# Kernel tuning notes

Measured on AMD Instinct MI355X. Metric: run time of the kernel, lower is better.

## Reference

```python
import jax, jax.numpy as jnp
import numpy as np

EPS = 0.001  # numerical_stabilizer


def setup_inputs() -> dict:
    key = jax.random.key(0)
    ks = jax.random.split(key, 8)
    B, L, D, H, M = 4, 4096, 1024, 16, 64
    scale = 0.02
    return {
        "query": jax.random.normal(ks[0], (B, L, D), jnp.float32),
        "key": jax.random.normal(ks[1], (B, L, D), jnp.float32),
        "value": jax.random.normal(ks[2], (B, L, D), jnp.float32),
        "Wq": jax.random.normal(ks[3], (D, H, M), jnp.float32) * scale,
        "bq": jnp.zeros((H, M), jnp.float32),
        "Wk": jax.random.normal(ks[4], (D, H, M), jnp.float32) * scale,
        "bk": jnp.zeros((H, M), jnp.float32),
        "Wv": jax.random.normal(ks[5], (D, H, M), jnp.float32) * scale,
        "bv": jnp.zeros((H, M), jnp.float32),
        "Wo": jax.random.normal(ks[6], (H, M, D), jnp.float32) * scale,
        "bo": jnp.zeros((D,), jnp.float32),
        "step": 0,
    }


def reference(query, key, value, Wq, bq, Wk, bk, Wv, bv, Wo, bo, step):
    # QKV projections: [B,L,D] x [D,H,M] -> [B,L,H,M]
    q = jnp.einsum('bld,dhm->blhm', query, Wq) + bq
    k = jnp.einsum('bld,dhm->blhm', key, Wk) + bk
    v = jnp.einsum('bld,dhm->blhm', value, Wv) + bv
    # ReLU feature map with stabilizer
    q = jax.nn.relu(q) + EPS
    k = jax.nn.relu(k) + EPS
    # Linear (kernelized) attention: KV outer-product state [B,H,M,M]
    kvs = jnp.einsum('blhm,blhd->bhmd', k, v)
    a_v = jnp.einsum('blhm,bhmd->blhd', q, kvs)
    # Normalizer: sum of keys over sequence
    ks_sum = jnp.sum(k, axis=1)                       # [B,H,M]
    norm = jnp.einsum('blhm,bhm->blh', q, ks_sum)     # [B,L,H]
    a_v = a_v / norm[..., None]
    # Output projection over (head, head_dim) -> hidden
    out = jnp.einsum('blhm,hmd->bld', a_v, Wo) + bo
    return out
```

## Files before the change

kernel.cpp:

```cpp
#include <hip/hip_runtime.h>
#include <stdint.h>


typedef __bf16 bf16;
typedef __bf16 bf16x4 __attribute__((ext_vector_type(4)));
typedef __bf16 bf16x8 __attribute__((ext_vector_type(8)));
typedef float f32x4 __attribute__((ext_vector_type(4)));

#define MFMA_(a, b, c) __builtin_amdgcn_mfma_f32_16x16x32_bf16((a), (b), (c), 0, 0, 0)

static constexpr int BB   = 4;
static constexpr int LSEQ = 4096;
static constexpr int DIM  = 1024;
static constexpr int HH   = 16;
static constexpr float EPSF = 0.001f;

__device__ __forceinline__ void gload16(bf16* lds, const bf16* g) {
  __builtin_amdgcn_global_load_lds(
      (const __attribute__((address_space(1))) void*)g,
      (__attribute__((address_space(3))) void*)lds, 16, 0, 0);
}

__global__ void k_prep_w4(const float* __restrict__ W0, const float* __restrict__ W1,
                          const float* __restrict__ W2, const float* __restrict__ W3,
                          bf16* __restrict__ T0, bf16* __restrict__ T1,
                          bf16* __restrict__ T2, bf16* __restrict__ T3) {
  const float* W; bf16* T;
  switch (blockIdx.z) {
    case 0:  W = W0; T = T0; break;
    case 1:  W = W1; T = T1; break;
    case 2:  W = W2; T = T2; break;
    default: W = W3; T = T3; break;
  }
  __shared__ float t[32][33];
  const int tx = threadIdx.x & 31, ty = threadIdx.x >> 5;
  const int r0 = blockIdx.x * 32, c0 = blockIdx.y * 32;
#pragma unroll
  for (int j = 0; j < 32; j += 8)
    t[ty + j][tx] = W[(size_t)(r0 + ty + j) * DIM + c0 + tx];
  __syncthreads();
#pragma unroll
  for (int j = 0; j < 32; j += 8)
    T[(size_t)(c0 + ty + j) * DIM + r0 + tx] = (bf16)t[tx][ty + j];
}

__global__ void k_init_vt(bf16* __restrict__ vt) {
  const int c = blockIdx.x * 256 + threadIdx.x;
  const int l8 = c & 511;
  const int r  = (c >> 9) & 15;
  const int bh = c >> 13;
  const bf16 val = (r == 0) ? (bf16)1.0f : (bf16)0.0f;
  bf16x8 o;
#pragma unroll
  for (int j = 0; j < 8; ++j) o[j] = val;
  *reinterpret_cast<bf16x8*>(vt + ((size_t)bh * 80 + 64 + r) * LSEQ + l8 * 8) = o;
}

template <int MODE>
__global__ __launch_bounds__(512, 2) void k_projf(const float* __restrict__ X,
                                                  const bf16* __restrict__ WT,
                                                  const float* __restrict__ bias,
                                                  bf16* __restrict__ outp) {
  __shared__ __align__(16) bf16 SH[65536];
  bf16* As = SH;
  bf16* Bs = SH + 16384;
  const int tid = threadIdx.x;
  const int lane = tid & 63, w = tid >> 6;
  const int wm = w >> 2, wn = w & 3;
  const int lr = lane & 15, lk = (lane >> 4) & 3;
  const int n0 = blockIdx.x * 256, c0 = blockIdx.y * 256;
  const int swz = (lr & 7) * 8;
  const int col0 = (lk * 8) ^ swz;
  const int col1 = (lk * 8 + 32) ^ swz;
  const int srow = lane >> 3;
  const int scol = (((lane & 7) ^ ((lane >> 3) & 7)) * 8);
  const float* Xb = X + (size_t)n0 * DIM;
  const bf16* Bb = WT + (size_t)c0 * DIM;

  f32x4 acc[8][4] = {};
  f32x4 af[8];
  const int arow[1] = {0};  (void)arow;

#pragma unroll
  for (int j = 0; j < 8; ++j) {
    const int idx = tid + j * 512, row = idx >> 4, c4 = idx & 15;
    af[j] = __builtin_nontemporal_load(
        reinterpret_cast<const f32x4*>(Xb + (size_t)row * DIM + c4 * 4));
  }

  for (int ks = 0; ks < 16; ++ks) {
    const int k0 = ks * 64;
    __syncthreads();
#pragma unroll
    for (int rr = 0; rr < 4; ++rr) {
      const int row = (rr * 8 + w) * 8 + srow;
      gload16(Bs + (rr * 8 + w) * 512, Bb + (size_t)row * DIM + k0 + scol);
    }
#pragma unroll
    for (int j = 0; j < 8; ++j) {
      const int idx = tid + j * 512, row = idx >> 4, c4 = idx & 15;
      bf16x4 o;
      o[0] = (bf16)af[j][0]; o[1] = (bf16)af[j][1];
      o[2] = (bf16)af[j][2]; o[3] = (bf16)af[j][3];
      *reinterpret_cast<bf16x4*>(
          &As[row * 64 + ((((c4 >> 1) ^ (row & 7)) << 3) | ((c4 & 1) << 2))]) = o;
    }
    __syncthreads();
    if (ks < 15) {
#pragma unroll
      for (int j = 0; j < 8; ++j) {
        const int idx = tid + j * 512, row = idx >> 4, c4 = idx & 15;
        af[j] = __builtin_nontemporal_load(
            reinterpret_cast<const f32x4*>(Xb + (size_t)row * DIM + k0 + 64 + c4 * 4));
      }
    }
    bf16x8 a[8][2], b[4][2];
#pragma unroll
    for (int f = 0; f < 8; ++f) {
      a[f][0] = *reinterpret_cast<const bf16x8*>(&As[(wm * 128 + f * 16 + lr) * 64 + col0]);
      a[f][1] = *reinterpret_cast<const bf16x8*>(&As[(wm * 128 + f * 16 + lr) * 64 + col1]);
    }
#pragma unroll
    for (int cb = 0; cb < 4; ++cb) {
      b[cb][0] = *reinterpret_cast<const bf16x8*>(&Bs[(wn * 64 + cb * 16 + lr) * 64 + col0]);
      b[cb][1] = *reinterpret_cast<const bf16x8*>(&Bs[(wn * 64 + cb * 16 + lr) * 64 + col1]);
    }
#pragma unroll
    for (int kk = 0; kk < 2; ++kk)
#pragma unroll
      for (int f = 0; f < 8; ++f)
#pragma unroll
        for (int cb = 0; cb < 4; ++cb)
          acc[f][cb] = MFMA_(a[f][kk], b[cb][kk], acc[f][cb]);
  }

  float bvv[4];
#pragma unroll
  for (int cb = 0; cb < 4; ++cb) bvv[cb] = bias[c0 + wn * 64 + cb * 16 + lr];
  const int bidx = n0 >> 12;
  const int l0 = n0 & (LSEQ - 1);

  if (MODE == 0) {
    __syncthreads();
#pragma unroll
    for (int f = 0; f < 8; ++f)
#pragma unroll
      for (int cb = 0; cb < 4; ++cb) {
        const int cl = wn * 64 + cb * 16 + lr;
#pragma unroll
        for (int r = 0; r < 4; ++r) {
          float x = acc[f][cb][r] + bvv[cb];
          x = fmaxf(x, 0.f) + EPSF;
          const int ll = wm * 128 + f * 16 + lk * 4 + r;
          SH[ll * 256 + ((((cl >> 3) ^ (ll & 7)) << 3) | (cl & 7))] = (bf16)x;
        }
      }
    __syncthreads();
#pragma unroll
    for (int it = 0; it < 16; ++it) {
      const int chunk = it * 512 + tid;
      const int row = chunk >> 5, blk = chunk & 31;
      const bf16x8 v = *reinterpret_cast<const bf16x8*>(&SH[row * 256 + ((blk ^ (row & 7)) << 3)]);
      *reinterpret_cast<bf16x8*>(outp + (size_t)(n0 + row) * DIM + c0 + blk * 8) = v;
    }
  } else {
    __syncthreads();
#pragma unroll
    for (int f = 0; f < 8; ++f)
#pragma unroll
      for (int cb = 0; cb < 4; ++cb) {
        const int cl = wn * 64 + cb * 16 + lr;
        const int ll = wm * 128 + f * 16 + lk * 4;
        bf16x4 o;
#pragma unroll
        for (int r = 0; r < 4; ++r) {
          float x = acc[f][cb][r] + bvv[cb];
          if (MODE == 1) x = fmaxf(x, 0.f) + EPSF;
          o[r] = (bf16)x;
        }
        *reinterpret_cast<bf16x4*>(
            &SH[cl * 256 + ((((ll >> 3) ^ (cl & 7)) << 3) | (ll & 7))]) = o;
      }
    __syncthreads();
#pragma unroll
    for (int it = 0; it < 16; ++it) {
      const int chunk = it * 512 + tid;
      const int row = chunk >> 5, blk = chunk & 31;
      const bf16x8 v = *reinterpret_cast<const bf16x8*>(&SH[row * 256 + ((blk ^ (row & 7)) << 3)]);
      const int cg = c0 + row;
      size_t rowbase;
      if (MODE == 1) rowbase = (size_t)bidx * 1024 + cg;
      else           rowbase = ((size_t)(bidx * HH + (cg >> 6)) * 80 + (cg & 63));
      *reinterpret_cast<bf16x8*>(outp + rowbase * LSEQ + l0 + blk * 8) = v;
    }
  }
}

__device__ __forceinline__ void stage_half(bf16* As0, bf16* Bs0,
                                           const bf16* Ab, const bf16* Bb,
                                           int h, int w, int srow, int scol) {
  const int t = h >> 2, reg = h & 3, buf = t & 1;
  bf16* lds = ((reg < 2) ? As0 : Bs0) + buf * 16384 + (reg & 1) * 8192;
  const bf16* g = (reg < 2) ? Ab : Bb;
  const int rbase = (reg & 1) * 128;
#pragma unroll
  for (int rr = 0; rr < 2; ++rr) {
    const int row = rbase + (rr * 8 + w) * 8 + srow;
    gload16(lds + (rr * 8 + w) * 512, g + (size_t)row * DIM + t * 64 + scol);
  }
}

#define LDA(d, g, f)                                                                              \
  a[d][0] = *reinterpret_cast<const bf16x8*>(&As0[(g) * 16384 + (wm * 128 + (f) * 16 + lr) * 64 + col0]); \
  a[d][1] = *reinterpret_cast<const bf16x8*>(&As0[(g) * 16384 + (wm * 128 + (f) * 16 + lr) * 64 + col1]);
#define LDB(d, g, c)                                                                              \
  b[d][0] = *reinterpret_cast<const bf16x8*>(&Bs0[(g) * 16384 + (wn * 64 + (c) * 16 + lr) * 64 + col0]); \
  b[d][1] = *reinterpret_cast<const bf16x8*>(&Bs0[(g) * 16384 + (wn * 64 + (c) * 16 + lr) * 64 + col1]);
#define MM(fi, ci, fo, co)                                                                        \
  acc[fo][co] = MFMA_(a[fi][0], b[ci][0], acc[fo][co]);                                           \
  acc[fo][co] = MFMA_(a[fi][1], b[ci][1], acc[fo][co]);

#define PHASE(g, q, pidx)                                                                         \
  {                                                                                               \
    if ((q) == 0) { LDA(0, g, 0) LDA(1, g, 1) LDA(2, g, 2) LDA(3, g, 3)                           \
                    LDB(0, g, 0) LDB(1, g, 1) }                                                   \
    else if ((q) == 1) { LDB(0, g, 2) LDB(1, g, 3) }                                              \
    else if ((q) == 2) { LDA(0, g, 4) LDA(1, g, 5) LDA(2, g, 6) LDA(3, g, 7) }                    \
    else { LDB(0, g, 0) LDB(1, g, 1) }                                                            \
    const int hh = 8 * i + 5 + (pidx);                                                            \
    if (hh < 64) stage_half(As0, Bs0, Ab, Bb, hh, w, srow, scol);                                 \
    if ((pidx) == 3 || (pidx) == 7) {                                                             \
      if (i < 7) { asm volatile("s_waitcnt vmcnt(2)" ::: "memory"); }                             \
      else       { asm volatile("s_waitcnt vmcnt(0)" ::: "memory"); }                             \
    }                                                                                             \
    __builtin_amdgcn_sched_barrier(0);                                                            \
    __builtin_amdgcn_s_barrier();                                                                 \
    __builtin_amdgcn_sched_barrier(0);                                                            \
    __builtin_amdgcn_s_setprio(1);                                                                \
    if ((q) == 0) { MM(0, 0, 0, 0) MM(1, 0, 1, 0) MM(2, 0, 2, 0) MM(3, 0, 3, 0)                   \
                    MM(0, 1, 0, 1) MM(1, 1, 1, 1) MM(2, 1, 2, 1) MM(3, 1, 3, 1) }                 \
    else if ((q) == 1) { MM(0, 0, 0, 2) MM(1, 0, 1, 2) MM(2, 0, 2, 2) MM(3, 0, 3, 2)              \
                         MM(0, 1, 0, 3) MM(1, 1, 1, 3) MM(2, 1, 2, 3) MM(3, 1, 3, 3) }            \
    else if ((q) == 2) { MM(0, 0, 4, 2) MM(1, 0, 5, 2) MM(2, 0, 6, 2) MM(3, 0, 7, 2)              \
                         MM(0, 1, 4, 3) MM(1, 1, 5, 3) MM(2, 1, 6, 3) MM(3, 1, 7, 3) }            \
    else { MM(0, 0, 4, 0) MM(1, 0, 5, 0) MM(2, 0, 6, 0) MM(3, 0, 7, 0)                            \
           MM(0, 1, 4, 1) MM(1, 1, 5, 1) MM(2, 1, 6, 1) MM(3, 1, 7, 1) }                          \
    __builtin_amdgcn_s_setprio(0);                                                                \
    __builtin_amdgcn_sched_barrier(0);                                                            \
    __builtin_amdgcn_s_barrier();                                                                 \
    __builtin_amdgcn_sched_barrier(0);                                                            \
  }

__global__ __launch_bounds__(512, 2) void k_gemm256(const bf16* __restrict__ X,
                                                    const bf16* __restrict__ WT,
                                                    const float* __restrict__ bias,
                                                    float* __restrict__ outp) {
  __shared__ __align__(16) bf16 SH[65536];
  bf16* As0 = SH;
  bf16* Bs0 = SH + 32768;
  const int tid = threadIdx.x;
  const int lane = tid & 63, w = tid >> 6;
  const int wm = w >> 2, wn = w & 3;
  const int lr = lane & 15, lk = (lane >> 4) & 3;
  const int n0 = blockIdx.x * 256, c0 = blockIdx.y * 256;
  const int swz = (lr & 7) * 8;
  const int col0 = (lk * 8) ^ swz;
  const int col1 = (lk * 8 + 32) ^ swz;
  const int srow = lane >> 3;
  const int scol = (((lane & 7) ^ ((lane >> 3) & 7)) * 8);
  const bf16* Ab = X + (size_t)n0 * DIM;
  const bf16* Bb = WT + (size_t)c0 * DIM;

  f32x4 acc[8][4] = {};
  bf16x8 a[4][2], b[2][2];

#pragma unroll
  for (int h = 0; h < 5; ++h) stage_half(As0, Bs0, Ab, Bb, h, w, srow, scol);
  asm volatile("s_waitcnt vmcnt(2)" ::: "memory");
  __builtin_amdgcn_sched_barrier(0);
  __builtin_amdgcn_s_barrier();
  __builtin_amdgcn_sched_barrier(0);

  for (int i = 0; i < 8; ++i) {
    PHASE(0, 0, 0) PHASE(0, 1, 1) PHASE(0, 2, 2) PHASE(0, 3, 3)
    PHASE(1, 0, 4) PHASE(1, 1, 5) PHASE(1, 2, 6) PHASE(1, 3, 7)
  }

  float bvv[4];
#pragma unroll
  for (int cb = 0; cb < 4; ++cb) bvv[cb] = bias[c0 + wn * 64 + cb * 16 + lr];
#pragma unroll
  for (int f = 0; f < 8; ++f)
#pragma unroll
    for (int cb = 0; cb < 4; ++cb) {
      const int c = c0 + wn * 64 + cb * 16 + lr;
#pragma unroll
      for (int r = 0; r < 4; ++r) {
        const int row = n0 + wm * 128 + f * 16 + lk * 4 + r;
        outp[(size_t)row * DIM + c] = acc[f][cb][r] + bvv[cb];
      }
    }
}
#undef PHASE
#undef MM
#undef LDB
#undef LDA

__global__ __launch_bounds__(256, 2) void k_kvs(const bf16* __restrict__ kt,
                                                const bf16* __restrict__ vt,
                                                float* __restrict__ kvs) {
  const int tid = threadIdx.x, lane = tid & 63, wid = tid >> 6;
  const int lr = lane & 15, lk = lane >> 4;
  const int bh = blockIdx.y;
  const int lbase = blockIdx.x * 256;
  __shared__ bf16 As[64][64];
  __shared__ bf16 Bs[80][64];
  f32x4 acc[5] = {};
  const bf16* ktb = kt + (size_t)bh * 64 * LSEQ;
  const bf16* vtb = vt + (size_t)bh * 80 * LSEQ;

  for (int ks = 0; ks < 4; ++ks) {
    const int l0 = lbase + ks * 64;
    __syncthreads();
#pragma unroll
    for (int i = 0; i < 2; ++i) {
      const int e = i * 2048 + tid * 8;
      const int row = e >> 6, col = e & 63;
      *reinterpret_cast<bf16x8*>(&As[row][col]) =
          *reinterpret_cast<const bf16x8*>(ktb + (size_t)row * LSEQ + l0 + col);
    }
#pragma unroll
    for (int i = 0; i < 2; ++i) {
      const int e = i * 2048 + tid * 8;
      const int row = e >> 6, col = e & 63;
      *reinterpret_cast<bf16x8*>(&Bs[row][col]) =
          *reinterpret_cast<const bf16x8*>(vtb + (size_t)row * LSEQ + l0 + col);
    }
    if (tid < 128) {
      const int e = 4096 + tid * 8;
      const int row = e >> 6, col = e & 63;
      *reinterpret_cast<bf16x8*>(&Bs[row][col]) =
          *reinterpret_cast<const bf16x8*>(vtb + (size_t)row * LSEQ + l0 + col);
    }
    __syncthreads();
#pragma unroll
    for (int kk = 0; kk < 2; ++kk) {
      const bf16x8 af = *reinterpret_cast<const bf16x8*>(&As[wid * 16 + lr][kk * 32 + lk * 8]);
#pragma unroll
      for (int cb = 0; cb < 5; ++cb) {
        const bf16x8 bfr = *reinterpret_cast<const bf16x8*>(&Bs[cb * 16 + lr][kk * 32 + lk * 8]);
        acc[cb] = MFMA_(af, bfr, acc[cb]);
      }
    }
  }
  float* kb = kvs + (size_t)bh * 64 * 80;
#pragma unroll
  for (int cb = 0; cb < 5; ++cb) {
    const int dcol = cb * 16 + lr;
#pragma unroll
    for (int r = 0; r < 4; ++r) {
      const int m = wid * 16 + lk * 4 + r;
      atomicAdd(kb + m * 80 + dcol, acc[cb][r]);
    }
  }
}

__global__ void k_kvs_t(const float* __restrict__ kvs, bf16* __restrict__ bav) {
  const int bh = blockIdx.x;
  const float* src = kvs + (size_t)bh * 5120;
  bf16* dst = bav + (size_t)bh * 5120;
  for (int i = threadIdx.x; i < 5120; i += 256) {
    const int dp = i >> 6, mm = i & 63;
    dst[i] = (bf16)src[mm * 80 + dp];
  }
}

__global__ __launch_bounds__(256, 2) void k_av(const bf16* __restrict__ q,
                                               const bf16* __restrict__ bav,
                                               bf16* __restrict__ avn) {
  const int tid = threadIdx.x, lane = tid & 63, wid = tid >> 6;
  const int lr = lane & 15, lk = lane >> 4;
  const int bh = blockIdx.y, b = bh >> 4, h = bh & 15;
  const int l0 = blockIdx.x * 128;
  __shared__ bf16 As[128][64];
  __shared__ bf16 Bs[80][64];
  __shared__ float nrm[128];

  const bf16* qb = q + ((size_t)b * LSEQ + l0) * DIM + h * 64;
#pragma unroll
  for (int i = 0; i < 4; ++i) {
    const int e = i * 2048 + tid * 8;
    const int row = e >> 6, col = e & 63;
    *reinterpret_cast<bf16x8*>(&As[row][col]) =
        *reinterpret_cast<const bf16x8*>(qb + (size_t)row * DIM + col);
  }
  const bf16* bb = bav + (size_t)bh * 5120;
#pragma unroll
  for (int i = 0; i < 2; ++i) {
    const int e = i * 2048 + tid * 8;
    const int row = e >> 6, col = e & 63;
    *reinterpret_cast<bf16x8*>(&Bs[row][col]) =
        *reinterpret_cast<const bf16x8*>(bb + row * 64 + col);
  }
  if (tid < 128) {
    const int e = 4096 + tid * 8;
    const int row = e >> 6, col = e & 63;
    *reinterpret_cast<bf16x8*>(&Bs[row][col]) =
        *reinterpret_cast<const bf16x8*>(bb + row * 64 + col);
  }
  __syncthreads();

  f32x4 acc[2][5] = {};
#pragma unroll
  for (int kk = 0; kk < 2; ++kk) {
    bf16x8 af[2];
    af[0] = *reinterpret_cast<const bf16x8*>(&As[wid * 32 + lr][kk * 32 + lk * 8]);
    af[1] = *reinterpret_cast<const bf16x8*>(&As[wid * 32 + 16 + lr][kk * 32 + lk * 8]);
#pragma unroll
    for (int cb = 0; cb < 5; ++cb) {
      const bf16x8 bfr = *reinterpret_cast<const bf16x8*>(&Bs[cb * 16 + lr][kk * 32 + lk * 8]);
      acc[0][cb] = MFMA_(af[0], bfr, acc[0][cb]);
      acc[1][cb] = MFMA_(af[1], bfr, acc[1][cb]);
    }
  }
  if (lr == 0) {
#pragma unroll
    for (int rb = 0; rb < 2; ++rb)
#pragma unroll
      for (int r = 0; r < 4; ++r)
        nrm[wid * 32 + rb * 16 + lk * 4 + r] = acc[rb][4][r];
  }
  __syncthreads();
  bf16* ob = avn + ((size_t)b * LSEQ + l0) * DIM + h * 64;
#pragma unroll
  for (int rb = 0; rb < 2; ++rb) {
#pragma unroll
    for (int cb = 0; cb < 4; ++cb) {
#pragma unroll
      for (int r = 0; r < 4; ++r) {
        const int row = wid * 32 + rb * 16 + lk * 4 + r;
        const float x = acc[rb][cb][r] / nrm[row];
        ob[(size_t)row * DIM + cb * 16 + lr] = (bf16)x;
      }
    }
  }
}

extern "C" void kernel_launch(void* const* d_in, const int* in_sizes, int n_in,
                              void* d_out, int out_size, void* d_ws, size_t ws_size,
                              hipStream_t stream) {
  const float* query = (const float*)d_in[0];
  const float* key   = (const float*)d_in[1];
  const float* value = (const float*)d_in[2];
  const float* Wq    = (const float*)d_in[3];
  const float* bq    = (const float*)d_in[4];
  const float* Wk    = (const float*)d_in[5];
  const float* bk    = (const float*)d_in[6];
  const float* Wv    = (const float*)d_in[7];
  const float* bvp   = (const float*)d_in[8];
  const float* Wo    = (const float*)d_in[9];
  const float* bo    = (const float*)d_in[10];
  float* out = (float*)d_out;
  char* ws = (char*)d_ws;

  const size_t off_wqt = 0;
  const size_t off_wkt = off_wqt + (2u << 20);
  const size_t off_wvt = off_wkt + (2u << 20);
  const size_t off_wot = off_wvt + (2u << 20);
  const size_t off_kt  = off_wot + (2u << 20);
  const size_t off_qb  = off_kt  + 33554432ull;
  const size_t off_av  = off_qb  + 33554432ull;
  const size_t off_vt  = off_av  + 33554432ull;
  const size_t off_kvs = off_vt  + 41943040ull;
  const size_t off_bav = off_kvs + 1310720ull;
  const size_t total   = off_bav + 655360ull;
  if (ws_size < total) return;

  bf16*  WQT = (bf16*)(ws + off_wqt);
  bf16*  WKT = (bf16*)(ws + off_wkt);
  bf16*  WVT = (bf16*)(ws + off_wvt);
  bf16*  WOT = (bf16*)(ws + off_wot);
  bf16*  KT  = (bf16*)(ws + off_kt);
  bf16*  Qb  = (bf16*)(ws + off_qb);
  bf16*  AV  = (bf16*)(ws + off_av);
  bf16*  VT  = (bf16*)(ws + off_vt);
  float* KVS = (float*)(ws + off_kvs);
  bf16*  BAV = (bf16*)(ws + off_bav);

  k_prep_w4<<<dim3(32, 32, 4), 256, 0, stream>>>(Wq, Wk, Wv, Wo, WQT, WKT, WVT, WOT);
  k_init_vt<<<2048, 256, 0, stream>>>(VT);
  (void)hipMemsetAsync(KVS, 0, 1310720ull, stream);

  k_projf<2><<<dim3(64, 4), 512, 0, stream>>>(value, WVT, bvp, VT);
  k_projf<1><<<dim3(64, 4), 512, 0, stream>>>(key,   WKT, bk, KT);
  k_projf<0><<<dim3(64, 4), 512, 0, stream>>>(query, WQT, bq, Qb);

  k_kvs<<<dim3(16, 64), 256, 0, stream>>>(KT, VT, KVS);
  k_kvs_t<<<64, 256, 0, stream>>>(KVS, BAV);

  k_av<<<dim3(32, 64), 256, 0, stream>>>(Qb, BAV, AV);

  k_gemm256<<<dim3(64, 4), 512, 0, stream>>>(AV, WOT, bo, out);
}
```

Measured before the change: 251.7 us.

## Merge Q/K/V projections into one launch with halved LDS epilogue

Replaces three separate projection kernel launches of 256 blocks each with a single 768-block launch that picks Q, K or V by blockIdx.z. This gives the GPU more concurrent blocks than a 256-block launch can provide. The LDS footprint is halved by writing the epilogue in two passes of 128 rows each, and launch bounds are raised to 4 blocks per CU to allow higher occupancy. Non-temporal loads on the fp32 inputs are replaced with ordinary loads. The risks are register pressure under the tighter launch bounds and the extra barrier in the epilogue.

```diff
diff --git a/kernel.cpp b/kernel.cpp
--- a/kernel.cpp
+++ b/kernel.cpp
@@ -56,14 +56,20 @@
   *reinterpret_cast<bf16x8*>(vt + ((size_t)bh * 80 + 64 + r) * LSEQ + l8 * 8) = o;
 }
 
-template <int MODE>
-__global__ __launch_bounds__(512, 2) void k_projf(const float* __restrict__ X,
-                                                  const bf16* __restrict__ WT,
-                                                  const float* __restrict__ bias,
-                                                  bf16* __restrict__ outp) {
-  __shared__ __align__(16) bf16 SH[65536];
+__global__ __launch_bounds__(512, 4) void k_proj3(
+    const float* __restrict__ Xq, const float* __restrict__ Xk, const float* __restrict__ Xv,
+    const bf16* __restrict__ WQT, const bf16* __restrict__ WKT, const bf16* __restrict__ WVT,
+    const float* __restrict__ bq, const float* __restrict__ bk, const float* __restrict__ bv,
+    bf16* __restrict__ Qb, bf16* __restrict__ KT, bf16* __restrict__ VT) {
+  __shared__ __align__(16) bf16 SH[32768];
   bf16* As = SH;
   bf16* Bs = SH + 16384;
+  const int mode = blockIdx.z;
+  const float* X    = (mode == 0) ? Xq  : (mode == 1) ? Xk  : Xv;
+  const bf16*  WT   = (mode == 0) ? WQT : (mode == 1) ? WKT : WVT;
+  const float* bias = (mode == 0) ? bq  : (mode == 1) ? bk  : bv;
+  bf16*        outp = (mode == 0) ? Qb  : (mode == 1) ? KT  : VT;
+
   const int tid = threadIdx.x;
   const int lane = tid & 63, w = tid >> 6;
   const int wm = w >> 2, wn = w & 3;
@@ -79,13 +85,11 @@
 
   f32x4 acc[8][4] = {};
   f32x4 af[8];
-  const int arow[1] = {0};  (void)arow;
 
 #pragma unroll
   for (int j = 0; j < 8; ++j) {
     const int idx = tid + j * 512, row = idx >> 4, c4 = idx & 15;
-    af[j] = __builtin_nontemporal_load(
-        reinterpret_cast<const f32x4*>(Xb + (size_t)row * DIM + c4 * 4));
+    af[j] = *reinterpret_cast<const f32x4*>(Xb + (size_t)row * DIM + c4 * 4);
   }
 
   for (int ks = 0; ks < 16; ++ks) {
@@ -110,8 +114,7 @@
 #pragma unroll
       for (int j = 0; j < 8; ++j) {
         const int idx = tid + j * 512, row = idx >> 4, c4 = idx & 15;
-        af[j] = __builtin_nontemporal_load(
-            reinterpret_cast<const f32x4*>(Xb + (size_t)row * DIM + k0 + 64 + c4 * 4));
+        af[j] = *reinterpret_cast<const f32x4*>(Xb + (size_t)row * DIM + k0 + 64 + c4 * 4);
       }
     }
     bf16x8 a[8][2], b[4][2];
@@ -140,58 +143,68 @@
   const int bidx = n0 >> 12;
   const int l0 = n0 & (LSEQ - 1);
 
-  if (MODE == 0) {
-    __syncthreads();
-#pragma unroll
-    for (int f = 0; f < 8; ++f)
-#pragma unroll
-      for (int cb = 0; cb < 4; ++cb) {
-        const int cl = wn * 64 + cb * 16 + lr;
-#pragma unroll
-        for (int r = 0; r < 4; ++r) {
-          float x = acc[f][cb][r] + bvv[cb];
-          x = fmaxf(x, 0.f) + EPSF;
-          const int ll = wm * 128 + f * 16 + lk * 4 + r;
-          SH[ll * 256 + ((((cl >> 3) ^ (ll & 7)) << 3) | (cl & 7))] = (bf16)x;
-        }
-      }
-    __syncthreads();
-#pragma unroll
-    for (int it = 0; it < 16; ++it) {
-      const int chunk = it * 512 + tid;
-      const int row = chunk >> 5, blk = chunk & 31;
-      const bf16x8 v = *reinterpret_cast<const bf16x8*>(&SH[row * 256 + ((blk ^ (row & 7)) << 3)]);
-      *reinterpret_cast<bf16x8*>(outp + (size_t)(n0 + row) * DIM + c0 + blk * 8) = v;
+  if (mode == 0) {
+#pragma unroll
+    for (int p = 0; p < 2; ++p) {
+      __syncthreads();
+      if (wm == p) {
+#pragma unroll
+        for (int f = 0; f < 8; ++f)
+#pragma unroll
+          for (int cb = 0; cb < 4; ++cb) {
+            const int cl = wn * 64 + cb * 16 + lr;
+#pragma unroll
+            for (int r = 0; r < 4; ++r) {
+              float x = acc[f][cb][r] + bvv[cb];
+              x = fmaxf(x, 0.f) + EPSF;
+              const int ll = f * 16 + lk * 4 + r;
+              SH[ll * 256 + ((((cl >> 3) ^ (ll & 7)) << 3) | (cl & 7))] = (bf16)x;
+            }
+          }
+      }
+      __syncthreads();
+#pragma unroll
+      for (int it = 0; it < 8; ++it) {
+        const int chunk = it * 512 + tid;
+        const int row = chunk >> 5, blk = chunk & 31;
+        const bf16x8 v = *reinterpret_cast<const bf16x8*>(&SH[row * 256 + ((blk ^ (row & 7)) << 3)]);
+        *reinterpret_cast<bf16x8*>(outp + (size_t)(n0 + p * 128 + row) * DIM + c0 + blk * 8) = v;
+      }
     }
   } else {
-    __syncthreads();
-#pragma unroll
-    for (int f = 0; f < 8; ++f)
-#pragma unroll
-      for (int cb = 0; cb < 4; ++cb) {
-        const int cl = wn * 64 + cb * 16 + lr;
-        const int ll = wm * 128 + f * 16 + lk * 4;
-        bf16x4 o;
-#pragma unroll
-        for (int r = 0; r < 4; ++r) {
-          float x = acc[f][cb][r] + bvv[cb];
-          if (MODE == 1) x = fmaxf(x, 0.f) + EPSF;
-          o[r] = (bf16)x;
-        }
-        *reinterpret_cast<bf16x4*>(
-            &SH[cl * 256 + ((((ll >> 3) ^ (cl & 7)) << 3) | (ll & 7))]) = o;
-      }
-    __syncthreads();
-#pragma unroll
-    for (int it = 0; it < 16; ++it) {
-      const int chunk = it * 512 + tid;
-      const int row = chunk >> 5, blk = chunk & 31;
-      const bf16x8 v = *reinterpret_cast<const bf16x8*>(&SH[row * 256 + ((blk ^ (row & 7)) << 3)]);
-      const int cg = c0 + row;
-      size_t rowbase;
-      if (MODE == 1) rowbase = (size_t)bidx * 1024 + cg;
-      else           rowbase = ((size_t)(bidx * HH + (cg >> 6)) * 80 + (cg & 63));
-      *reinterpret_cast<bf16x8*>(outp + rowbase * LSEQ + l0 + blk * 8) = v;
+#pragma unroll
+    for (int p = 0; p < 2; ++p) {
+      __syncthreads();
+      if (wm == p) {
+#pragma unroll
+        for (int f = 0; f < 8; ++f)
+#pragma unroll
+          for (int cb = 0; cb < 4; ++cb) {
+            const int cl = wn * 64 + cb * 16 + lr;
+            const int ll = f * 16 + lk * 4;
+            bf16x4 o;
+#pragma unroll
+            for (int r = 0; r < 4; ++r) {
+              float x = acc[f][cb][r] + bvv[cb];
+              if (mode == 1) x = fmaxf(x, 0.f) + EPSF;
+              o[r] = (bf16)x;
+            }
+            *reinterpret_cast<bf16x4*>(
+                &SH[cl * 128 + ((((ll >> 3) ^ (cl & 7)) << 3) | (ll & 7))]) = o;
+          }
+      }
+      __syncthreads();
+#pragma unroll
+      for (int it = 0; it < 8; ++it) {
+        const int chunk = it * 512 + tid;
+        const int row = chunk >> 4, blk = chunk & 15;
+        const bf16x8 v = *reinterpret_cast<const bf16x8*>(&SH[row * 128 + ((blk ^ (row & 7)) << 3)]);
+        const int cg = c0 + row;
+        size_t rowbase;
+        if (mode == 1) rowbase = (size_t)bidx * 1024 + cg;
+        else           rowbase = ((size_t)(bidx * HH + (cg >> 6)) * 80 + (cg & 63));
+        *reinterpret_cast<bf16x8*>(outp + rowbase * LSEQ + l0 + p * 128 + blk * 8) = v;
+      }
     }
   }
 }
@@ -491,9 +504,10 @@
   k_init_vt<<<2048, 256, 0, stream>>>(VT);
   (void)hipMemsetAsync(KVS, 0, 1310720ull, stream);
 
-  k_projf<2><<<dim3(64, 4), 512, 0, stream>>>(value, WVT, bvp, VT);
-  k_projf<1><<<dim3(64, 4), 512, 0, stream>>>(key,   WKT, bk, KT);
-  k_projf<0><<<dim3(64, 4), 512, 0, stream>>>(query, WQT, bq, Qb);
+  k_proj3<<<dim3(64, 4, 3), 512, 0, stream>>>(query, key, value,
+                                              WQT, WKT, WVT,
+                                              bq, bk, bvp,
+                                              Qb, KT, VT);
 
   k_kvs<<<dim3(16, 64), 256, 0, stream>>>(KT, VT, KVS);
   k_kvs_t<<<64, 256, 0, stream>>>(KVS, BAV);
```

New measurement: 1.005 ms. 299% more time.
